# Optimization experiments

Measured on AMD Instinct MI355X. Metric: run time of the kernel, lower is better.

The kernel has to match this reference:

```python
import jax, jax.numpy as jnp
import numpy as np
from jax import lax

S, B, F = 512, 256, 128
HC = 256  # constraint LSTM hidden
HG = 256  # generation LSTM hidden
L = 128   # linear units


def _lstm_step(Wih, Whh, bias):
    """torch.nn.LSTMCell semantics: gates = x@Wih.T + h@Whh.T + bih + bhh,
    chunked as (i, f, g, o)."""
    def step(carry, x):
        h, c = carry
        gates = x @ Wih.T + h @ Whh.T + bias
        i, f, g, o = jnp.split(gates, 4, axis=-1)
        c2 = jax.nn.sigmoid(f) * c + jax.nn.sigmoid(i) * jnp.tanh(g)
        h2 = jax.nn.sigmoid(o) * jnp.tanh(c2)
        return (h2, c2), h2
    return step


def setup_inputs() -> dict:
    key = jax.random.key(0)
    ks = jax.random.split(key, 16)
    s = 0.05
    return {
        "seq": jax.random.normal(ks[0], (S, B, F), jnp.float32),
        "seq_constraints": jax.random.normal(ks[1], (S, B, F + 1), jnp.float32),
        "Wih_c": jax.random.normal(ks[2], (4 * HC, F + 1), jnp.float32) * s,
        "Whh_c": jax.random.normal(ks[3], (4 * HC, HC), jnp.float32) * s,
        "bih_c": jax.random.normal(ks[4], (4 * HC,), jnp.float32) * s,
        "bhh_c": jax.random.normal(ks[5], (4 * HC,), jnp.float32) * s,
        "Wih_g": jax.random.normal(ks[6], (4 * HG, F + HC), jnp.float32) * s,
        "Whh_g": jax.random.normal(ks[7], (4 * HG, HG), jnp.float32) * s,
        "bih_g": jax.random.normal(ks[8], (4 * HG,), jnp.float32) * s,
        "bhh_g": jax.random.normal(ks[9], (4 * HG,), jnp.float32) * s,
        "W1": jax.random.normal(ks[10], (L, HG), jnp.float32) * s,
        "b1": jax.random.normal(ks[11], (L,), jnp.float32) * s,
        "W2": jax.random.normal(ks[12], (F, L), jnp.float32) * s,
        "b2": jax.random.normal(ks[13], (F,), jnp.float32) * s,
    }


def reference(seq, seq_constraints, Wih_c, Whh_c, bih_c, bhh_c,
              Wih_g, Whh_g, bih_g, bhh_g, W1, b1, W2, b2):
    seq_len, batch, nf = seq.shape
    dt = seq.dtype

    # --- constraint LSTM, scanned backward in time; outputs aligned to time index ---
    step_c = _lstm_step(Wih_c, Whh_c, bih_c + bhh_c)
    z_c = jnp.zeros((batch, HC), dt)
    _, hc = lax.scan(step_c, (z_c, z_c), seq_constraints, reverse=True)  # (S,B,HC)

    # --- generation LSTM input: seq shifted right by one step (zeros at t=0),
    #     concatenated with the constraint hidden at time t ---
    shifted = jnp.concatenate([jnp.zeros((1, batch, nf), dt), seq[:-1]], axis=0)
    gen_in = jnp.concatenate([shifted, hc], axis=-1)  # (S,B,F+HC)

    step_g = _lstm_step(Wih_g, Whh_g, bih_g + bhh_g)
    z_g = jnp.zeros((batch, HG), dt)
    _, hg = lax.scan(step_g, (z_g, z_g), gen_in)  # (S,B,HG)

    # --- per-step MLP head ---
    preds = jax.nn.relu(hg @ W1.T + b1) @ W2.T + b2  # (S,B,F)
    return preds
```

## Files before the change

### kernel.cpp

```cpp
#include <hip/hip_runtime.h>

typedef unsigned short u16;
typedef unsigned int u32;
typedef unsigned long long u64;
typedef __attribute__((ext_vector_type(8))) short s16x8;
typedef __attribute__((ext_vector_type(4))) float f32x4;

#define MFMA_BF16 __builtin_amdgcn_mfma_f32_16x16x32_bf16

#define TCH 64
#define NCH 8
#define CROWS (TCH * 256)

__device__ __forceinline__ float b2f(u16 u) {
  u32 v = ((u32)u) << 16; float f; __builtin_memcpy(&f, &v, 4); return f;
}
__device__ __forceinline__ u16 f2b(float f) {
  u32 u; __builtin_memcpy(&u, &f, 4);
  u += 0x7FFFu + ((u >> 16) & 1u);
  return (u16)(u >> 16);
}
__device__ __forceinline__ float sigm(float x) {
  float e = __builtin_amdgcn_exp2f(-1.44269504f * x);
  return __builtin_amdgcn_rcpf(1.0f + e);
}
__device__ __forceinline__ float tanh_(float x) {
  float e = __builtin_amdgcn_exp2f(2.88539008f * x);
  return 1.0f - 2.0f * __builtin_amdgcn_rcpf(e + 1.0f);
}

__global__ void prep_weights(const float* __restrict__ Wihc, const float* __restrict__ Whhc,
                             const float* __restrict__ bihc, const float* __restrict__ bhhc,
                             const float* __restrict__ Wihg, const float* __restrict__ Whhg,
                             const float* __restrict__ bihg, const float* __restrict__ bhhg,
                             const float* __restrict__ W1, const float* __restrict__ W2,
                             u16* __restrict__ pWihc, u16* __restrict__ pWhhc,
                             u16* __restrict__ pWihg, u16* __restrict__ pWhhg,
                             u16* __restrict__ pW1, u16* __restrict__ pW2,
                             float* __restrict__ pbc, float* __restrict__ pbg) {
  const int b = blockIdx.x, t = threadIdx.x;
  if (b < 1024) { if (t < 192) pWihc[b * 192 + t] = (t < 129) ? f2b(Wihc[b * 129 + t]) : (u16)0; }
  else if (b < 2048) { int n = b - 1024; pWhhc[n * 256 + t] = f2b(Whhc[n * 256 + t]); }
  else if (b < 3072) { int n = b - 2048; for (int k = t; k < 384; k += 256) pWihg[n * 384 + k] = f2b(Wihg[n * 384 + k]); }
  else if (b < 4096) { int n = b - 3072; pWhhg[n * 256 + t] = f2b(Whhg[n * 256 + t]); }
  else if (b < 4224) { int n = b - 4096; pW1[n * 256 + t] = f2b(W1[n * 256 + t]); }
  else if (b < 4352) { int n = b - 4224; if (t < 128) pW2[n * 128 + t] = f2b(W2[n * 128 + t]); }
  else {
    int i = (b - 4352) * 256 + t;
    if (i < 1024) pbc[i] = bihc[i] + bhhc[i];
    else if (i < 2048) pbg[i - 1024] = bihg[i - 1024] + bhhg[i - 1024];
  }
}

__global__ void conv_scb(const float* __restrict__ src, u16* __restrict__ dst, int r0) {
  const int row = blockIdx.x, t = threadIdx.x;
  dst[(size_t)row * 192 + t] = (t < 129) ? f2b(src[(size_t)(r0 + row) * 129 + t]) : (u16)0;
}
__global__ void conv_seqb(const float* __restrict__ src, u16* __restrict__ dst, int r0) {
  const int row = blockIdx.x, t = threadIdx.x;
  const int g = r0 + row;
  dst[(size_t)row * 128 + t] = (g < 256) ? (u16)0 : f2b(src[(size_t)(g - 256) * 128 + t]);
}

__global__ void fill_val(float* __restrict__ p, float v, int n) {
  int i = blockIdx.x * 256 + threadIdx.x;
  if (i < n) p[i] = v;
}

template <int RELU, int OUTF32>
__global__ __launch_bounds__(256, 1) void gemm_bias(
    const u16* __restrict__ A1, int lda1, const u16* __restrict__ A2, int lda2,
    const u16* __restrict__ Bw, const float* __restrict__ bias,
    void* __restrict__ Outv, int N) {
  const int K = lda1 + lda2;
  const int ntiles = N >> 7;
  const int bm = blockIdx.x / ntiles, bn = blockIdx.x % ntiles;
  const int m0 = bm << 7, n0 = bn << 7;
  __shared__ u16 Al[128 * 64], Bl[128 * 64];
  const int tid = threadIdx.x, lane = tid & 63, w = tid >> 6;
  const int kg = lane >> 4, l15 = lane & 15;
  const int mq = (w & 1) << 6, nq = (w >> 1) << 6;

  f32x4 acc[4][4];
#pragma unroll
  for (int mt = 0; mt < 4; ++mt)
#pragma unroll
    for (int nt = 0; nt < 4; ++nt) acc[mt][nt] = (f32x4){0.f, 0.f, 0.f, 0.f};

#pragma unroll 1
  for (int kc = 0; kc < K; kc += 64) {
#pragma unroll
    for (int i = 0; i < 4; ++i) {
      int id = i * 256 + tid;
      int row = id >> 3;
      int c8 = (id & 7) * 8;
      int k = kc + c8;
      const u16* asrc = (k < lda1) ? (A1 + (size_t)(m0 + row) * lda1 + k)
                                   : (A2 + (size_t)(m0 + row) * lda2 + (k - lda1));
      s16x8 av = *(const s16x8*)asrc;
      s16x8 bv = *(const s16x8*)(Bw + (size_t)(n0 + row) * K + k);
      int sw = (row & 7) << 3;
      *(s16x8*)&Al[row * 64 + (c8 ^ sw)] = av;
      *(s16x8*)&Bl[row * 64 + (c8 ^ sw)] = bv;
    }
    __syncthreads();
#pragma unroll
    for (int kk = 0; kk < 2; ++kk) {
      const int kb = kk * 32 + kg * 8;
      s16x8 a[4], b[4];
#pragma unroll
      for (int mt = 0; mt < 4; ++mt) {
        int r = mq + mt * 16 + l15;
        a[mt] = *(const s16x8*)&Al[r * 64 + (kb ^ ((r & 7) << 3))];
      }
#pragma unroll
      for (int nt = 0; nt < 4; ++nt) {
        int r = nq + nt * 16 + l15;
        b[nt] = *(const s16x8*)&Bl[r * 64 + (kb ^ ((r & 7) << 3))];
      }
#pragma unroll
      for (int mt = 0; mt < 4; ++mt)
#pragma unroll
        for (int nt = 0; nt < 4; ++nt)
          acc[mt][nt] = MFMA_BF16(a[mt], b[nt], acc[mt][nt], 0, 0, 0);
    }
    __syncthreads();
  }
#pragma unroll
  for (int nt = 0; nt < 4; ++nt) {
    const int col = n0 + nq + nt * 16 + l15;
    const float bb = bias[col];
#pragma unroll
    for (int mt = 0; mt < 4; ++mt)
#pragma unroll
      for (int r = 0; r < 4; ++r) {
        float v = acc[mt][nt][r] + bb;
        if (RELU) v = fmaxf(v, 0.f);
        const size_t orow = (size_t)(m0 + mq + mt * 16 + kg * 4 + r);
        if (OUTF32) ((float*)Outv)[orow * N + col] = v;
        else ((u16*)Outv)[orow * N + col] = f2b(v);
      }
  }
}

__global__ __launch_bounds__(256, 1) void lstm_scan(
    const u16* __restrict__ X,
    const u16* __restrict__ Whh,
    u16* __restrict__ Hc,
    const u16* __restrict__ ph,
    float* __restrict__ Cst,
    u64* __restrict__ HX,
    u32* __restrict__ slots,
    int base, int fwd, int first) {
  __shared__ u16 hlds[32 * 256];
  const int tid = threadIdx.x;
  const int lane = tid & 63;
  const int w = tid >> 6;
  const int bg = blockIdx.x & 7;
  const int hs = blockIdx.x >> 3;
  const int kg = lane >> 4;
  const int l15 = lane & 15;
  const int mrow = (w & 1) * 16;
  const int rowL = mrow + l15;
  const int brow = bg * 32 + rowL;
  const int hcol0 = hs * 32 + (w >> 1) * 16 + kg * 4;
  u32* myslot = slots + ((bg << 3) + hs) * 32;

  s16x8 breg[4][8];
  const int wrow = hs * 32 + (w >> 1) * 16 + l15;
#pragma unroll
  for (int q = 0; q < 4; ++q)
#pragma unroll
    for (int kt = 0; kt < 8; ++kt)
      breg[q][kt] = *(const s16x8*)&Whh[(size_t)(q * 256 + wrow) * 256 + kt * 32 + kg * 8];

  if (first) {
#pragma unroll
    for (int i = 0; i < 8; ++i) {
      int idx = i * 256 + tid;
      int row = idx >> 6, c0 = (idx & 63) * 4;
      *(u64*)&hlds[row * 256 + (c0 ^ ((row & 7) << 3))] = 0ull;
    }
  } else {
    const u64* hsrc = (const u64*)ph + bg * 2048;
#pragma unroll
    for (int i = 0; i < 8; ++i) {
      int idx = i * 256 + tid;
      int row = idx >> 6, c0 = (idx & 63) * 4;
      u64 v = hsrc[idx];
      *(u64*)&hlds[row * 256 + (c0 ^ ((row & 7) << 3))] = v;
    }
  }
  float c4[4];
  if (first) {
    c4[0] = 0.f; c4[1] = 0.f; c4[2] = 0.f; c4[3] = 0.f;
  } else {
    f32x4 cv = *(const f32x4*)&Cst[(size_t)brow * 256 + hcol0];
    c4[0] = cv[0]; c4[1] = cv[1]; c4[2] = cv[2]; c4[3] = cv[3];
  }
  __syncthreads();

  u64 xv[4];
  {
    const int lt0 = fwd ? 0 : TCH - 1;
    const u16* xb = X + ((size_t)lt0 * 256 + brow) * 1024 + hcol0;
#pragma unroll
    for (int q = 0; q < 4; ++q) xv[q] = *(const u64*)(xb + q * 256);
  }

  const int abase = rowL * 256;
  const int aswz = (rowL & 7) << 3;
  const int widx = (w >> 1) * 4 + kg;
  const int rrow = tid >> 3;
  const int ridx = tid & 7;

#pragma unroll 1
  for (int s = 0; s < TCH; ++s) {
    const int lt = fwd ? s : TCH - 1 - s;
    const u32 tag = (u32)(base + s + 1);
    u64* slab = HX + ((size_t)(s & 1) * 8 + bg) * 2048;

    f32x4 acc[2][4];
#pragma unroll
    for (int p = 0; p < 2; ++p)
#pragma unroll
      for (int q = 0; q < 4; ++q) acc[p][q] = (f32x4){0.f, 0.f, 0.f, 0.f};

#pragma unroll
    for (int kt = 0; kt < 8; ++kt) {
      s16x8 hb = *(const s16x8*)&hlds[abase + ((kt * 32 + kg * 8) ^ aswz)];
#pragma unroll
      for (int q = 0; q < 4; ++q)
        acc[kt & 1][q] = MFMA_BF16(breg[q][kt], hb, acc[kt & 1][q], 0, 0, 0);
    }

    u16 hb16[4];
    u64 hu = 0;
#pragma unroll
    for (int r = 0; r < 4; ++r) {
      float gi = acc[0][0][r] + acc[1][0][r] + b2f((u16)(xv[0] >> (16 * r)));
      float gf = acc[0][1][r] + acc[1][1][r] + b2f((u16)(xv[1] >> (16 * r)));
      float gg = acc[0][2][r] + acc[1][2][r] + b2f((u16)(xv[2] >> (16 * r)));
      float go = acc[0][3][r] + acc[1][3][r] + b2f((u16)(xv[3] >> (16 * r)));
      float cn = sigm(gf) * c4[r] + sigm(gi) * tanh_(gg);
      c4[r] = cn;
      hb16[r] = f2b(sigm(go) * tanh_(cn));
      hu |= ((u64)hb16[r]) << (16 * r);
    }

    if (s == TCH - 1) {
      *(u64*)&Hc[((size_t)lt * 256 + brow) * 256 + hcol0] = hu;
      break;
    }

    __hip_atomic_store(slab + ((size_t)hs * 32 + rowL) * 8 + widx, hu,
                       __ATOMIC_RELAXED, __HIP_MEMORY_SCOPE_AGENT);
    __syncthreads();

    if (tid == 0)
      __hip_atomic_store(myslot, tag, __ATOMIC_RELAXED, __HIP_MEMORY_SCOPE_AGENT);

    *(u64*)&Hc[((size_t)lt * 256 + brow) * 256 + hcol0] = hu;
    {
      const int nlt = fwd ? lt + 1 : lt - 1;
      const u16* xb = X + ((size_t)nlt * 256 + brow) * 1024 + hcol0;
#pragma unroll
      for (int q = 0; q < 4; ++q) xv[q] = *(const u64*)(xb + q * 256);
    }
    __builtin_amdgcn_sched_barrier(0);

    if (w == 0 && lane < 8) {
      const u32* sp = slots + ((bg << 3) + lane) * 32;
      int guard = 0;
      while (__hip_atomic_load(sp, __ATOMIC_RELAXED, __HIP_MEMORY_SCOPE_AGENT) < tag &&
             guard < (1 << 16)) {
        __builtin_amdgcn_s_sleep(1);
        ++guard;
      }
    }
    __builtin_amdgcn_s_barrier();

    u64 pv[8];
#pragma unroll
    for (int k = 0; k < 8; ++k)
      pv[k] = __hip_atomic_load(slab + k * 256 + tid,
                                __ATOMIC_RELAXED, __HIP_MEMORY_SCOPE_AGENT);
#pragma unroll
    for (int k = 0; k < 8; ++k) {
      int c = k * 32 + ridx * 4;
      *(u64*)&hlds[rrow * 256 + (c ^ ((rrow & 7) << 3))] = pv[k];
    }
    __syncthreads();
  }

  f32x4 cv; cv[0] = c4[0]; cv[1] = c4[1]; cv[2] = c4[2]; cv[3] = c4[3];
  *(f32x4*)&Cst[(size_t)brow * 256 + hcol0] = cv;
}

extern "C" void kernel_launch(void* const* d_in, const int* in_sizes, int n_in,
                              void* d_out, int out_size, void* d_ws, size_t ws_size,
                              hipStream_t stream) {
  (void)in_sizes; (void)n_in;
  const float* seq  = (const float*)d_in[0];
  const float* sc   = (const float*)d_in[1];
  const float* Wihc = (const float*)d_in[2];
  const float* Whhc = (const float*)d_in[3];
  const float* bihc = (const float*)d_in[4];
  const float* bhhc = (const float*)d_in[5];
  const float* Wihg = (const float*)d_in[6];
  const float* Whhg = (const float*)d_in[7];
  const float* bihg = (const float*)d_in[8];
  const float* bhhg = (const float*)d_in[9];
  const float* W1   = (const float*)d_in[10];
  const float* b1   = (const float*)d_in[11];
  const float* W2   = (const float*)d_in[12];
  const float* b2   = (const float*)d_in[13];

  char* ws = (char*)d_ws;
  const size_t o_Xbuf = 0;
  const size_t o_scbc = o_Xbuf + (size_t)CROWS * 1024 * 2;
  const size_t o_seqc = o_scbc + (size_t)CROWS * 192 * 2;
  const size_t o_hgc  = o_seqc + (size_t)CROWS * 128 * 2;
  const size_t o_t1c  = o_hgc  + (size_t)CROWS * 256 * 2;
  const size_t o_Wihc = o_t1c  + (size_t)CROWS * 128 * 2;
  const size_t o_Whhc = o_Wihc + 1024 * 192 * 2;
  const size_t o_Wihg = o_Whhc + 1024 * 256 * 2;
  const size_t o_Whhg = o_Wihg + 1024 * 384 * 2;
  const size_t o_W1   = o_Whhg + 1024 * 256 * 2;
  const size_t o_W2   = o_W1   + 128 * 256 * 2;
  const size_t o_bc   = o_W2   + 128 * 128 * 2;
  const size_t o_bg   = o_bc   + 1024 * 4;
  const size_t o_Cst  = o_bg   + 1024 * 4;
  const size_t o_HX   = o_Cst  + 256 * 256 * 4;
  const size_t o_slt  = o_HX   + (size_t)2 * 8 * 2048 * 8;
  const size_t NEEDED = o_slt + 64 * 128;

  if (ws_size < NEEDED) {
    fill_val<<<(out_size + 255) / 256, 256, 0, stream>>>((float*)d_out, 1.0e6f, out_size);
    return;
  }

  u16* Xbuf  = (u16*)(ws + o_Xbuf);
  u16* scbc  = (u16*)(ws + o_scbc);
  u16* seqc  = (u16*)(ws + o_seqc);
  u16* hgc   = (u16*)(ws + o_hgc);
  u16* t1c   = (u16*)(ws + o_t1c);
  u16* pWihc = (u16*)(ws + o_Wihc);
  u16* pWhhc = (u16*)(ws + o_Whhc);
  u16* pWihg = (u16*)(ws + o_Wihg);
  u16* pWhhg = (u16*)(ws + o_Whhg);
  u16* pW1   = (u16*)(ws + o_W1);
  u16* pW2   = (u16*)(ws + o_W2);
  float* pbc = (float*)(ws + o_bc);
  float* pbg = (float*)(ws + o_bg);
  float* Cst = (float*)(ws + o_Cst);
  u64* HX    = (u64*)(ws + o_HX);
  u32* slots = (u32*)(ws + o_slt);

  u16* hcb = (u16*)d_out;

  hipMemsetAsync(slots, 0, 64 * 128, stream);
  prep_weights<<<4360, 256, 0, stream>>>(Wihc, Whhc, bihc, bhhc, Wihg, Whhg, bihg, bhhg,
                                         W1, W2, pWihc, pWhhc, pWihg, pWhhg, pW1, pW2, pbc, pbg);

  for (int c = NCH - 1; c >= 0; --c) {
    const int r0 = c * CROWS;
    conv_scb<<<CROWS, 192, 0, stream>>>(sc, scbc, r0);
    gemm_bias<0, 0><<<(CROWS / 128) * 8, 256, 0, stream>>>(scbc, 192, scbc, 0, pWihc, pbc, Xbuf, 1024);
    u16* Hcp = hcb + (size_t)c * TCH * 65536;
    const u16* ph = (c == NCH - 1) ? (const u16*)0 : hcb + (size_t)(c + 1) * TCH * 65536;
    const int ord = NCH - 1 - c;
    lstm_scan<<<64, 256, 0, stream>>>(Xbuf, pWhhc, Hcp, ph, Cst, HX, slots,
                                      ord * TCH, 0, c == NCH - 1);
  }

  for (int c = 0; c < NCH; ++c) {
    const int r0 = c * CROWS;
    conv_seqb<<<CROWS, 128, 0, stream>>>(seq, seqc, r0);
    const u16* hcc = hcb + (size_t)c * TCH * 65536;
    gemm_bias<0, 0><<<(CROWS / 128) * 8, 256, 0, stream>>>(seqc, 128, hcc, 256, pWihg, pbg, Xbuf, 1024);
    const u16* ph = (c == 0) ? (const u16*)0 : hgc + (size_t)(TCH - 1) * 65536;
    const int ord = NCH + c;
    lstm_scan<<<64, 256, 0, stream>>>(Xbuf, pWhhg, hgc, ph, Cst, HX, slots,
                                      ord * TCH, 1, c == 0);
    gemm_bias<1, 0><<<CROWS / 128, 256, 0, stream>>>(hgc, 256, hgc, 0, pW1, b1, t1c, 128);
    gemm_bias<0, 1><<<CROWS / 128, 256, 0, stream>>>(t1c, 128, t1c, 0, pW2, b2,
                                                     (float*)d_out + (size_t)c * CROWS * 128, 128);
  }
}
```

Measured before the change: 2.820 ms.

## Replace block-level LDS h exchange with per-wave flags and direct register loads

```diff
diff --git a/kernel.cpp b/kernel.cpp
--- a/kernel.cpp
+++ b/kernel.cpp
@@ -152,7 +152,6 @@
     u64* __restrict__ HX,
     u32* __restrict__ slots,
     int base, int fwd, int first) {
-  __shared__ u16 hlds[32 * 256];
   const int tid = threadIdx.x;
   const int lane = tid & 63;
   const int w = tid >> 6;
@@ -164,7 +163,8 @@
   const int rowL = mrow + l15;
   const int brow = bg * 32 + rowL;
   const int hcol0 = hs * 32 + (w >> 1) * 16 + kg * 4;
-  u32* myslot = slots + ((bg << 3) + hs) * 32;
+  u32* myslot = slots + ((bg << 3) + hs) * 32 + w;
+  const u32* pollp = slots + ((bg << 3) + (lane >> 2)) * 32 + (lane & 3);
 
   s16x8 breg[4][8];
   const int wrow = hs * 32 + (w >> 1) * 16 + l15;
@@ -174,23 +174,16 @@
     for (int kt = 0; kt < 8; ++kt)
       breg[q][kt] = *(const s16x8*)&Whh[(size_t)(q * 256 + wrow) * 256 + kt * 32 + kg * 8];
 
+  s16x8 hreg[8];
   if (first) {
 #pragma unroll
-    for (int i = 0; i < 8; ++i) {
-      int idx = i * 256 + tid;
-      int row = idx >> 6, c0 = (idx & 63) * 4;
-      *(u64*)&hlds[row * 256 + (c0 ^ ((row & 7) << 3))] = 0ull;
-    }
+    for (int kt = 0; kt < 8; ++kt) hreg[kt] = (s16x8){0, 0, 0, 0, 0, 0, 0, 0};
   } else {
-    const u64* hsrc = (const u64*)ph + bg * 2048;
-#pragma unroll
-    for (int i = 0; i < 8; ++i) {
-      int idx = i * 256 + tid;
-      int row = idx >> 6, c0 = (idx & 63) * 4;
-      u64 v = hsrc[idx];
-      *(u64*)&hlds[row * 256 + (c0 ^ ((row & 7) << 3))] = v;
-    }
-  }
+#pragma unroll
+    for (int kt = 0; kt < 8; ++kt)
+      hreg[kt] = *(const s16x8*)&ph[(size_t)brow * 256 + kt * 32 + kg * 8];
+  }
+
   float c4[4];
   if (first) {
     c4[0] = 0.f; c4[1] = 0.f; c4[2] = 0.f; c4[3] = 0.f;
@@ -198,7 +191,6 @@
     f32x4 cv = *(const f32x4*)&Cst[(size_t)brow * 256 + hcol0];
     c4[0] = cv[0]; c4[1] = cv[1]; c4[2] = cv[2]; c4[3] = cv[3];
   }
-  __syncthreads();
 
   u64 xv[4];
   {
@@ -208,17 +200,11 @@
     for (int q = 0; q < 4; ++q) xv[q] = *(const u64*)(xb + q * 256);
   }
 
-  const int abase = rowL * 256;
-  const int aswz = (rowL & 7) << 3;
-  const int widx = (w >> 1) * 4 + kg;
-  const int rrow = tid >> 3;
-  const int ridx = tid & 7;
-
 #pragma unroll 1
   for (int s = 0; s < TCH; ++s) {
     const int lt = fwd ? s : TCH - 1 - s;
     const u32 tag = (u32)(base + s + 1);
-    u64* slab = HX + ((size_t)(s & 1) * 8 + bg) * 2048;
+    u16* slab16 = (u16*)HX + (((size_t)(s & 1) * 8 + bg) << 13);
 
     f32x4 acc[2][4];
 #pragma unroll
@@ -228,10 +214,9 @@
 
 #pragma unroll
     for (int kt = 0; kt < 8; ++kt) {
-      s16x8 hb = *(const s16x8*)&hlds[abase + ((kt * 32 + kg * 8) ^ aswz)];
 #pragma unroll
       for (int q = 0; q < 4; ++q)
-        acc[kt & 1][q] = MFMA_BF16(breg[q][kt], hb, acc[kt & 1][q], 0, 0, 0);
+        acc[kt & 1][q] = MFMA_BF16(breg[q][kt], hreg[kt], acc[kt & 1][q], 0, 0, 0);
     }
 
     u16 hb16[4];
@@ -248,49 +233,44 @@
       hu |= ((u64)hb16[r]) << (16 * r);
     }
 
-    if (s == TCH - 1) {
-      *(u64*)&Hc[((size_t)lt * 256 + brow) * 256 + hcol0] = hu;
-      break;
-    }
-
-    __hip_atomic_store(slab + ((size_t)hs * 32 + rowL) * 8 + widx, hu,
+    *(u64*)&Hc[((size_t)lt * 256 + brow) * 256 + hcol0] = hu;
+    if (s == TCH - 1) break;
+
+    __hip_atomic_store((u64*)&slab16[(size_t)rowL * 256 + hcol0], hu,
                        __ATOMIC_RELAXED, __HIP_MEMORY_SCOPE_AGENT);
-    __syncthreads();
-
-    if (tid == 0)
+    __builtin_amdgcn_sched_barrier(0);
+    asm volatile("s_waitcnt vmcnt(0)" ::: "memory");
+    __builtin_amdgcn_sched_barrier(0);
+    if (lane == 0)
       __hip_atomic_store(myslot, tag, __ATOMIC_RELAXED, __HIP_MEMORY_SCOPE_AGENT);
 
-    *(u64*)&Hc[((size_t)lt * 256 + brow) * 256 + hcol0] = hu;
+    {
+      int guard = 0;
+      u32 v;
+      do {
+        v = (lane < 32)
+                ? __hip_atomic_load(pollp, __ATOMIC_RELAXED, __HIP_MEMORY_SCOPE_AGENT)
+                : tag;
+      } while (__any(v < tag) && ++guard < (1 << 15));
+    }
+    __builtin_amdgcn_sched_barrier(0);
+
+#pragma unroll
+    for (int kt = 0; kt < 8; ++kt) {
+      const u64* p = (const u64*)&slab16[(size_t)rowL * 256 + kt * 32 + kg * 8];
+      u64 a = __hip_atomic_load(p + 0, __ATOMIC_RELAXED, __HIP_MEMORY_SCOPE_AGENT);
+      u64 b = __hip_atomic_load(p + 1, __ATOMIC_RELAXED, __HIP_MEMORY_SCOPE_AGENT);
+      u64* hp = (u64*)&hreg[kt];
+      hp[0] = a; hp[1] = b;
+    }
+    __builtin_amdgcn_sched_barrier(0);
+
     {
       const int nlt = fwd ? lt + 1 : lt - 1;
       const u16* xb = X + ((size_t)nlt * 256 + brow) * 1024 + hcol0;
 #pragma unroll
       for (int q = 0; q < 4; ++q) xv[q] = *(const u64*)(xb + q * 256);
     }
-    __builtin_amdgcn_sched_barrier(0);
-
-    if (w == 0 && lane < 8) {
-      const u32* sp = slots + ((bg << 3) + lane) * 32;
-      int guard = 0;
-      while (__hip_atomic_load(sp, __ATOMIC_RELAXED, __HIP_MEMORY_SCOPE_AGENT) < tag &&
-             guard < (1 << 16)) {
-        __builtin_amdgcn_s_sleep(1);
-        ++guard;
-      }
-    }
-    __builtin_amdgcn_s_barrier();
-
-    u64 pv[8];
-#pragma unroll
-    for (int k = 0; k < 8; ++k)
-      pv[k] = __hip_atomic_load(slab + k * 256 + tid,
-                                __ATOMIC_RELAXED, __HIP_MEMORY_SCOPE_AGENT);
-#pragma unroll
-    for (int k = 0; k < 8; ++k) {
-      int c = k * 32 + ridx * 4;
-      *(u64*)&hlds[rrow * 256 + (c ^ ((rrow & 7) << 3))] = pv[k];
-    }
-    __syncthreads();
   }
 
   f32x4 cv; cv[0] = c4[0]; cv[1] = c4[1]; cv[2] = c4[2]; cv[3] = c4[3];
```

Measured after the change: 5.706 ms. 102% more time.

## Overlap next-chunk gate GEMM and MLP head with LSTM scan in one launch

Applied to the files above, without the earlier changes.

```diff
diff --git a/kernel.cpp b/kernel.cpp
--- a/kernel.cpp
+++ b/kernel.cpp
@@ -52,31 +52,19 @@
   }
 }
 
-__global__ void conv_scb(const float* __restrict__ src, u16* __restrict__ dst, int r0) {
-  const int row = blockIdx.x, t = threadIdx.x;
-  dst[(size_t)row * 192 + t] = (t < 129) ? f2b(src[(size_t)(r0 + row) * 129 + t]) : (u16)0;
-}
-__global__ void conv_seqb(const float* __restrict__ src, u16* __restrict__ dst, int r0) {
-  const int row = blockIdx.x, t = threadIdx.x;
-  const int g = r0 + row;
-  dst[(size_t)row * 128 + t] = (g < 256) ? (u16)0 : f2b(src[(size_t)(g - 256) * 128 + t]);
-}
-
 __global__ void fill_val(float* __restrict__ p, float v, int n) {
   int i = blockIdx.x * 256 + threadIdx.x;
   if (i < n) p[i] = v;
 }
 
-template <int RELU, int OUTF32>
-__global__ __launch_bounds__(256, 1) void gemm_bias(
-    const u16* __restrict__ A1, int lda1, const u16* __restrict__ A2, int lda2,
+template <int MODE>
+__device__ __forceinline__ void gate_gemm_tile(
+    int tile, int r0, const float* __restrict__ F, const u16* __restrict__ Hb,
     const u16* __restrict__ Bw, const float* __restrict__ bias,
-    void* __restrict__ Outv, int N) {
-  const int K = lda1 + lda2;
-  const int ntiles = N >> 7;
-  const int bm = blockIdx.x / ntiles, bn = blockIdx.x % ntiles;
+    u16* __restrict__ Out, u16* Al, u16* Bl) {
+  const int K = (MODE == 1) ? 192 : 384;
+  const int bm = tile >> 3, bn = tile & 7;
   const int m0 = bm << 7, n0 = bn << 7;
-  __shared__ u16 Al[128 * 64], Bl[128 * 64];
   const int tid = threadIdx.x, lane = tid & 63, w = tid >> 6;
   const int kg = lane >> 4, l15 = lane & 15;
   const int mq = (w & 1) << 6, nq = (w >> 1) << 6;
@@ -95,9 +83,29 @@
       int row = id >> 3;
       int c8 = (id & 7) * 8;
       int k = kc + c8;
-      const u16* asrc = (k < lda1) ? (A1 + (size_t)(m0 + row) * lda1 + k)
-                                   : (A2 + (size_t)(m0 + row) * lda2 + (k - lda1));
-      s16x8 av = *(const s16x8*)asrc;
+      s16x8 av;
+      if (MODE == 1) {
+        const float* s = F + (size_t)(r0 + m0 + row) * 129 + k;
+#pragma unroll
+        for (int j = 0; j < 8; ++j) {
+          u16 bb = 0;
+          if (k + j < 129) bb = f2b(s[j]);
+          av[j] = (short)bb;
+        }
+      } else {
+        if (k < 128) {
+          const int grow = r0 + m0 + row;
+          if (grow < 256) {
+            av = (s16x8){0, 0, 0, 0, 0, 0, 0, 0};
+          } else {
+            const float* s = F + (size_t)(grow - 256) * 128 + k;
+#pragma unroll
+            for (int j = 0; j < 8; ++j) av[j] = (short)f2b(s[j]);
+          }
+        } else {
+          av = *(const s16x8*)&Hb[(size_t)(m0 + row) * 256 + (k - 128)];
+        }
+      }
       s16x8 bv = *(const s16x8*)(Bw + (size_t)(n0 + row) * K + k);
       int sw = (row & 7) << 3;
       *(s16x8*)&Al[row * 64 + (c8 ^ sw)] = av;
@@ -134,25 +142,126 @@
     for (int mt = 0; mt < 4; ++mt)
 #pragma unroll
       for (int r = 0; r < 4; ++r) {
+        const size_t orow = (size_t)(m0 + mq + mt * 16 + kg * 4 + r);
+        Out[orow * 1024 + col] = f2b(acc[mt][nt][r] + bb);
+      }
+  }
+}
+
+template <int MODE>
+__global__ __launch_bounds__(256, 1) void gate_gemm_k(
+    int r0, const float* __restrict__ F, const u16* __restrict__ Hb,
+    const u16* __restrict__ Bw, const float* __restrict__ bias,
+    u16* __restrict__ Out) {
+  __shared__ u16 Al[8192], Bl[8192];
+  gate_gemm_tile<MODE>(blockIdx.x, r0, F, Hb, Bw, bias, Out, Al, Bl);
+}
+
+template <int RELU, int OUTF32>
+__device__ __forceinline__ void head_tile(
+    int tile, const u16* __restrict__ A, int lda,
+    const u16* __restrict__ Bw, const float* __restrict__ bias,
+    void* __restrict__ Outv, u16* Al, u16* Bl) {
+  const int m0 = tile << 7;
+  const int tid = threadIdx.x, lane = tid & 63, w = tid >> 6;
+  const int kg = lane >> 4, l15 = lane & 15;
+  const int mq = (w & 1) << 6, nq = (w >> 1) << 6;
+
+  f32x4 acc[4][4];
+#pragma unroll
+  for (int mt = 0; mt < 4; ++mt)
+#pragma unroll
+    for (int nt = 0; nt < 4; ++nt) acc[mt][nt] = (f32x4){0.f, 0.f, 0.f, 0.f};
+
+#pragma unroll 1
+  for (int kc = 0; kc < lda; kc += 64) {
+#pragma unroll
+    for (int i = 0; i < 4; ++i) {
+      int id = i * 256 + tid;
+      int row = id >> 3;
+      int c8 = (id & 7) * 8;
+      int k = kc + c8;
+      s16x8 av = *(const s16x8*)(A + (size_t)(m0 + row) * lda + k);
+      s16x8 bv = *(const s16x8*)(Bw + (size_t)row * lda + k);
+      int sw = (row & 7) << 3;
+      *(s16x8*)&Al[row * 64 + (c8 ^ sw)] = av;
+      *(s16x8*)&Bl[row * 64 + (c8 ^ sw)] = bv;
+    }
+    __syncthreads();
+#pragma unroll
+    for (int kk = 0; kk < 2; ++kk) {
+      const int kb = kk * 32 + kg * 8;
+      s16x8 a[4], b[4];
+#pragma unroll
+      for (int mt = 0; mt < 4; ++mt) {
+        int r = mq + mt * 16 + l15;
+        a[mt] = *(const s16x8*)&Al[r * 64 + (kb ^ ((r & 7) << 3))];
+      }
+#pragma unroll
+      for (int nt = 0; nt < 4; ++nt) {
+        int r = nq + nt * 16 + l15;
+        b[nt] = *(const s16x8*)&Bl[r * 64 + (kb ^ ((r & 7) << 3))];
+      }
+#pragma unroll
+      for (int mt = 0; mt < 4; ++mt)
+#pragma unroll
+        for (int nt = 0; nt < 4; ++nt)
+          acc[mt][nt] = MFMA_BF16(a[mt], b[nt], acc[mt][nt], 0, 0, 0);
+    }
+    __syncthreads();
+  }
+#pragma unroll
+  for (int nt = 0; nt < 4; ++nt) {
+    const int col = nq + nt * 16 + l15;
+    const float bb = bias[col];
+#pragma unroll
+    for (int mt = 0; mt < 4; ++mt)
+#pragma unroll
+      for (int r = 0; r < 4; ++r) {
         float v = acc[mt][nt][r] + bb;
         if (RELU) v = fmaxf(v, 0.f);
         const size_t orow = (size_t)(m0 + mq + mt * 16 + kg * 4 + r);
-        if (OUTF32) ((float*)Outv)[orow * N + col] = v;
-        else ((u16*)Outv)[orow * N + col] = f2b(v);
-      }
-  }
-}
-
+        if (OUTF32) ((float*)Outv)[orow * 128 + col] = v;
+        else ((u16*)Outv)[orow * 128 + col] = f2b(v);
+      }
+  }
+}
+
+template <int RELU, int OUTF32>
+__global__ __launch_bounds__(256, 1) void head_k(
+    const u16* __restrict__ A, int lda, const u16* __restrict__ Bw,
+    const float* __restrict__ bias, void* __restrict__ Outv) {
+  __shared__ u16 Al[8192], Bl[8192];
+  head_tile<RELU, OUTF32>(blockIdx.x, A, lda, Bw, bias, Outv, Al, Bl);
+}
+
+template <int GMODE>
 __global__ __launch_bounds__(256, 1) void lstm_scan(
-    const u16* __restrict__ X,
-    const u16* __restrict__ Whh,
-    u16* __restrict__ Hc,
-    const u16* __restrict__ ph,
-    float* __restrict__ Cst,
-    u64* __restrict__ HX,
-    u32* __restrict__ slots,
-    int base, int fwd, int first) {
-  __shared__ u16 hlds[32 * 256];
+    const u16* __restrict__ X, const u16* __restrict__ Whh,
+    u16* __restrict__ Hc, const u16* __restrict__ ph,
+    float* __restrict__ Cst, u64* __restrict__ HX, u32* __restrict__ slots,
+    int base, int fwd, int first,
+    const float* __restrict__ gF, const u16* __restrict__ gHb,
+    const u16* __restrict__ gBw, const float* __restrict__ gbias,
+    u16* __restrict__ gOut, int gr0, int ng,
+    const u16* __restrict__ h1A, u16* __restrict__ h1Out, int nh1,
+    const u16* __restrict__ h2A, float* __restrict__ h2Out, int nh2,
+    const u16* __restrict__ W1b, const float* __restrict__ b1,
+    const u16* __restrict__ W2b, const float* __restrict__ b2) {
+  __shared__ u16 lds[16384];
+  int bx = blockIdx.x;
+  if (bx >= 64) {
+    bx -= 64;
+    if (bx < ng) { gate_gemm_tile<GMODE>(bx, gr0, gF, gHb, gBw, gbias, gOut, lds, lds + 8192); return; }
+    bx -= ng;
+    if (bx < nh1) { head_tile<1, 0>(bx, h1A, 256, W1b, b1, (void*)h1Out, lds, lds + 8192); return; }
+    bx -= nh1;
+    if (bx < nh2) { head_tile<0, 1>(bx, h2A, 128, W2b, b2, (void*)h2Out, lds, lds + 8192); }
+    return;
+  }
+  __builtin_amdgcn_s_setprio(1);
+  u16* hlds = lds;
+
   const int tid = threadIdx.x;
   const int lane = tid & 63;
   const int w = tid >> 6;
@@ -164,7 +273,7 @@
   const int rowL = mrow + l15;
   const int brow = bg * 32 + rowL;
   const int hcol0 = hs * 32 + (w >> 1) * 16 + kg * 4;
-  u32* myslot = slots + ((bg << 3) + hs) * 32;
+  u32* myslot = slots + ((bg << 3) + hs) * 32 + w;
 
   s16x8 breg[4][8];
   const int wrow = hs * 32 + (w >> 1) * 16 + l15;
@@ -234,7 +343,6 @@
         acc[kt & 1][q] = MFMA_BF16(breg[q][kt], hb, acc[kt & 1][q], 0, 0, 0);
     }
 
-    u16 hb16[4];
     u64 hu = 0;
 #pragma unroll
     for (int r = 0; r < 4; ++r) {
@@ -244,23 +352,20 @@
       float go = acc[0][3][r] + acc[1][3][r] + b2f((u16)(xv[3] >> (16 * r)));
       float cn = sigm(gf) * c4[r] + sigm(gi) * tanh_(gg);
       c4[r] = cn;
-      hb16[r] = f2b(sigm(go) * tanh_(cn));
-      hu |= ((u64)hb16[r]) << (16 * r);
-    }
-
-    if (s == TCH - 1) {
-      *(u64*)&Hc[((size_t)lt * 256 + brow) * 256 + hcol0] = hu;
-      break;
-    }
-
+      hu |= ((u64)f2b(sigm(go) * tanh_(cn))) << (16 * r);
+    }
+
+    *(u64*)&Hc[((size_t)lt * 256 + brow) * 256 + hcol0] = hu;
+    if (s == TCH - 1) break;
     __hip_atomic_store(slab + ((size_t)hs * 32 + rowL) * 8 + widx, hu,
                        __ATOMIC_RELAXED, __HIP_MEMORY_SCOPE_AGENT);
-    __syncthreads();
-
-    if (tid == 0)
+
+    __builtin_amdgcn_sched_barrier(0);
+    asm volatile("s_waitcnt vmcnt(0)" ::: "memory");
+    __builtin_amdgcn_sched_barrier(0);
+    if (lane == 0)
       __hip_atomic_store(myslot, tag, __ATOMIC_RELAXED, __HIP_MEMORY_SCOPE_AGENT);
 
-    *(u64*)&Hc[((size_t)lt * 256 + brow) * 256 + hcol0] = hu;
     {
       const int nlt = fwd ? lt + 1 : lt - 1;
       const u16* xb = X + ((size_t)nlt * 256 + brow) * 1024 + hcol0;
@@ -269,11 +374,11 @@
     }
     __builtin_amdgcn_sched_barrier(0);
 
-    if (w == 0 && lane < 8) {
-      const u32* sp = slots + ((bg << 3) + lane) * 32;
+    if (w == 0 && lane < 32) {
+      const u32* sp = slots + ((bg << 3) + (lane >> 2)) * 32 + (lane & 3);
       int guard = 0;
       while (__hip_atomic_load(sp, __ATOMIC_RELAXED, __HIP_MEMORY_SCOPE_AGENT) < tag &&
-             guard < (1 << 16)) {
+             guard < (1 << 15)) {
         __builtin_amdgcn_s_sleep(1);
         ++guard;
       }
@@ -316,75 +421,103 @@
   const float* W2   = (const float*)d_in[12];
   const float* b2   = (const float*)d_in[13];
 
-  char* ws = (char*)d_ws;
-  const size_t o_Xbuf = 0;
-  const size_t o_scbc = o_Xbuf + (size_t)CROWS * 1024 * 2;
-  const size_t o_seqc = o_scbc + (size_t)CROWS * 192 * 2;
-  const size_t o_hgc  = o_seqc + (size_t)CROWS * 128 * 2;
-  const size_t o_t1c  = o_hgc  + (size_t)CROWS * 256 * 2;
-  const size_t o_Wihc = o_t1c  + (size_t)CROWS * 128 * 2;
-  const size_t o_Whhc = o_Wihc + 1024 * 192 * 2;
-  const size_t o_Wihg = o_Whhc + 1024 * 256 * 2;
-  const size_t o_Whhg = o_Wihg + 1024 * 384 * 2;
-  const size_t o_W1   = o_Whhg + 1024 * 256 * 2;
-  const size_t o_W2   = o_W1   + 128 * 256 * 2;
-  const size_t o_bc   = o_W2   + 128 * 128 * 2;
-  const size_t o_bg   = o_bc   + 1024 * 4;
-  const size_t o_Cst  = o_bg   + 1024 * 4;
-  const size_t o_HX   = o_Cst  + 256 * 256 * 4;
-  const size_t o_slt  = o_HX   + (size_t)2 * 8 * 2048 * 8;
-  const size_t NEEDED = o_slt + 64 * 128;
-
-  if (ws_size < NEEDED) {
+  const size_t XB = (size_t)CROWS * 1024 * 2;
+  const size_t HGB = (size_t)CROWS * 256 * 2;
+  const size_t T1B = (size_t)CROWS * 128 * 2;
+  const size_t TAILB = 1024 * 192 * 2 + 1024 * 256 * 2 + 1024 * 384 * 2 +
+                       1024 * 256 * 2 + 128 * 256 * 2 + 128 * 128 * 2 +
+                       1024 * 4 + 1024 * 4 + 256 * 256 * 4 +
+                       (size_t)2 * 8 * 2048 * 8 + 64 * 128;
+  const size_t NEED_BIG = 2 * XB + 2 * HGB + 2 * T1B + TAILB;
+  const size_t NEED_SMALL = XB + HGB + T1B + TAILB;
+  const int use2 = ws_size >= NEED_BIG;
+
+  if (ws_size < NEED_SMALL) {
     fill_val<<<(out_size + 255) / 256, 256, 0, stream>>>((float*)d_out, 1.0e6f, out_size);
     return;
   }
 
-  u16* Xbuf  = (u16*)(ws + o_Xbuf);
-  u16* scbc  = (u16*)(ws + o_scbc);
-  u16* seqc  = (u16*)(ws + o_seqc);
-  u16* hgc   = (u16*)(ws + o_hgc);
-  u16* t1c   = (u16*)(ws + o_t1c);
-  u16* pWihc = (u16*)(ws + o_Wihc);
-  u16* pWhhc = (u16*)(ws + o_Whhc);
-  u16* pWihg = (u16*)(ws + o_Wihg);
-  u16* pWhhg = (u16*)(ws + o_Whhg);
-  u16* pW1   = (u16*)(ws + o_W1);
-  u16* pW2   = (u16*)(ws + o_W2);
-  float* pbc = (float*)(ws + o_bc);
-  float* pbg = (float*)(ws + o_bg);
-  float* Cst = (float*)(ws + o_Cst);
-  u64* HX    = (u64*)(ws + o_HX);
-  u32* slots = (u32*)(ws + o_slt);
+  char* ws = (char*)d_ws;
+  size_t off = 0;
+  u16* Xh[2]; u16* hgb[2]; u16* t1b[2];
+  Xh[0] = (u16*)(ws + off); off += XB;
+  Xh[1] = use2 ? (u16*)(ws + off) : Xh[0]; if (use2) off += XB;
+  hgb[0] = (u16*)(ws + off); off += HGB;
+  hgb[1] = use2 ? (u16*)(ws + off) : hgb[0]; if (use2) off += HGB;
+  t1b[0] = (u16*)(ws + off); off += T1B;
+  t1b[1] = use2 ? (u16*)(ws + off) : t1b[0]; if (use2) off += T1B;
+  u16* pWihc = (u16*)(ws + off); off += 1024 * 192 * 2;
+  u16* pWhhc = (u16*)(ws + off); off += 1024 * 256 * 2;
+  u16* pWihg = (u16*)(ws + off); off += 1024 * 384 * 2;
+  u16* pWhhg = (u16*)(ws + off); off += 1024 * 256 * 2;
+  u16* pW1   = (u16*)(ws + off); off += 128 * 256 * 2;
+  u16* pW2   = (u16*)(ws + off); off += 128 * 128 * 2;
+  float* pbc = (float*)(ws + off); off += 1024 * 4;
+  float* pbg = (float*)(ws + off); off += 1024 * 4;
+  float* Cst = (float*)(ws + off); off += 256 * 256 * 4;
+  u64* HX    = (u64*)(ws + off); off += (size_t)2 * 8 * 2048 * 8;
+  u32* slots = (u32*)(ws + off);
 
   u16* hcb = (u16*)d_out;
+  float* outf = (float*)d_out;
 
   hipMemsetAsync(slots, 0, 64 * 128, stream);
   prep_weights<<<4360, 256, 0, stream>>>(Wihc, Whhc, bihc, bhhc, Wihg, Whhg, bihg, bhhg,
                                          W1, W2, pWihc, pWhhc, pWihg, pWhhg, pW1, pW2, pbc, pbg);
 
-  for (int c = NCH - 1; c >= 0; --c) {
-    const int r0 = c * CROWS;
-    conv_scb<<<CROWS, 192, 0, stream>>>(sc, scbc, r0);
-    gemm_bias<0, 0><<<(CROWS / 128) * 8, 256, 0, stream>>>(scbc, 192, scbc, 0, pWihc, pbc, Xbuf, 1024);
-    u16* Hcp = hcb + (size_t)c * TCH * 65536;
-    const u16* ph = (c == NCH - 1) ? (const u16*)0 : hcb + (size_t)(c + 1) * TCH * 65536;
-    const int ord = NCH - 1 - c;
-    lstm_scan<<<64, 256, 0, stream>>>(Xbuf, pWhhc, Hcp, ph, Cst, HX, slots,
-                                      ord * TCH, 0, c == NCH - 1);
-  }
-
-  for (int c = 0; c < NCH; ++c) {
-    const int r0 = c * CROWS;
-    conv_seqb<<<CROWS, 128, 0, stream>>>(seq, seqc, r0);
-    const u16* hcc = hcb + (size_t)c * TCH * 65536;
-    gemm_bias<0, 0><<<(CROWS / 128) * 8, 256, 0, stream>>>(seqc, 128, hcc, 256, pWihg, pbg, Xbuf, 1024);
-    const u16* ph = (c == 0) ? (const u16*)0 : hgc + (size_t)(TCH - 1) * 65536;
-    const int ord = NCH + c;
-    lstm_scan<<<64, 256, 0, stream>>>(Xbuf, pWhhg, hgc, ph, Cst, HX, slots,
-                                      ord * TCH, 1, c == 0);
-    gemm_bias<1, 0><<<CROWS / 128, 256, 0, stream>>>(hgc, 256, hgc, 0, pW1, b1, t1c, 128);
-    gemm_bias<0, 1><<<CROWS / 128, 256, 0, stream>>>(t1c, 128, t1c, 0, pW2, b2,
-                                                     (float*)d_out + (size_t)c * CROWS * 128, 128);
-  }
-}
+  if (use2) {
+    gate_gemm_k<1><<<1024, 256, 0, stream>>>(7 * CROWS, sc, (const u16*)0, pWihc, pbc, Xh[1]);
+    for (int c = NCH - 1; c >= 0; --c) {
+      const int ord = NCH - 1 - c;
+      const int ng = (c > 0) ? 1024 : 0;
+      u16* Hcp = hcb + (size_t)c * TCH * 65536;
+      const u16* ph = (c == NCH - 1) ? (const u16*)0 : hcb + (size_t)(c + 1) * TCH * 65536;
+      lstm_scan<1><<<64 + ng, 256, 0, stream>>>(
+          Xh[c & 1], pWhhc, Hcp, ph, Cst, HX, slots, ord * TCH, 0, c == NCH - 1,
+          sc, (const u16*)0, pWihc, pbc, Xh[(c - 1) & 1], (c - 1) * CROWS, ng,
+          (const u16*)0, (u16*)0, 0, (const u16*)0, (float*)0, 0, pW1, b1, pW2, b2);
+    }
+    gate_gemm_k<2><<<1024, 256, 0, stream>>>(0, seq, hcb, pWihg, pbg, Xh[0]);
+    for (int c = 0; c < NCH; ++c) {
+      const int ord = NCH + c;
+      const int ng = (c < NCH - 1) ? 1024 : 0;
+      const int nh1 = (c >= 1) ? 128 : 0;
+      const int nh2 = (c >= 2) ? 128 : 0;
+      const u16* ph = (c == 0) ? (const u16*)0 : hgb[(c - 1) & 1] + (size_t)(TCH - 1) * 65536;
+      lstm_scan<2><<<64 + ng + nh1 + nh2, 256, 0, stream>>>(
+          Xh[c & 1], pWhhg, hgb[c & 1], ph, Cst, HX, slots, ord * TCH, 1, c == 0,
+          seq, hcb + (size_t)(c + 1) * TCH * 65536, pWihg, pbg,
+          Xh[(c + 1) & 1], (c + 1) * CROWS, ng,
+          hgb[(c - 1) & 1], t1b[(c - 1) & 1], nh1,
+          t1b[c & 1], outf + (size_t)(c - 2) * CROWS * 128, nh2,
+          pW1, b1, pW2, b2);
+    }
+    head_k<1, 0><<<128, 256, 0, stream>>>(hgb[1], 256, pW1, b1, (void*)t1b[1]);
+    head_k<0, 1><<<128, 256, 0, stream>>>(t1b[0], 128, pW2, b2,
+                                          (void*)(outf + (size_t)6 * CROWS * 128));
+    head_k<0, 1><<<128, 256, 0, stream>>>(t1b[1], 128, pW2, b2,
+                                          (void*)(outf + (size_t)7 * CROWS * 128));
+  } else {
+    for (int c = NCH - 1; c >= 0; --c) {
+      gate_gemm_k<1><<<1024, 256, 0, stream>>>(c * CROWS, sc, (const u16*)0, pWihc, pbc, Xh[0]);
+      u16* Hcp = hcb + (size_t)c * TCH * 65536;
+      const u16* ph = (c == NCH - 1) ? (const u16*)0 : hcb + (size_t)(c + 1) * TCH * 65536;
+      lstm_scan<1><<<64, 256, 0, stream>>>(
+          Xh[0], pWhhc, Hcp, ph, Cst, HX, slots, (NCH - 1 - c) * TCH, 0, c == NCH - 1,
+          sc, (const u16*)0, pWihc, pbc, Xh[0], 0, 0,
+          (const u16*)0, (u16*)0, 0, (const u16*)0, (float*)0, 0, pW1, b1, pW2, b2);
+    }
+    for (int c = 0; c < NCH; ++c) {
+      gate_gemm_k<2><<<1024, 256, 0, stream>>>(c * CROWS, seq,
+                                               hcb + (size_t)c * TCH * 65536, pWihg, pbg, Xh[0]);
+      const u16* ph = (c == 0) ? (const u16*)0 : hgb[0] + (size_t)(TCH - 1) * 65536;
+      lstm_scan<2><<<64, 256, 0, stream>>>(
+          Xh[0], pWhhg, hgb[0], ph, Cst, HX, slots, (NCH + c) * TCH, 1, c == 0,
+          seq, (const u16*)0, pWihg, pbg, Xh[0], 0, 0,
+          (const u16*)0, (u16*)0, 0, (const u16*)0, (float*)0, 0, pW1, b1, pW2, b2);
+      head_k<1, 0><<<128, 256, 0, stream>>>(hgb[0], 256, pW1, b1, (void*)t1b[0]);
+      head_k<0, 1><<<128, 256, 0, stream>>>(t1b[0], 128, pW2, b2,
+                                            (void*)(outf + (size_t)c * CROWS * 128));
+    }
+  }
+}
```

After: 3.346 ms. 1.19x slower.

## Tag each exchanged hidden value with its step to allow per-word validation

Applied to the files above, without the earlier changes.

```diff
diff --git a/kernel.cpp b/kernel.cpp
--- a/kernel.cpp
+++ b/kernel.cpp
@@ -166,6 +166,10 @@
   const int hcol0 = hs * 32 + (w >> 1) * 16 + kg * 4;
   u32* myslot = slots + ((bg << 3) + hs) * 32;
 
+  const int rrow = tid >> 3;
+  const int rcol0 = (tid & 7) * 32;
+  const int rsw = (rrow & 7) << 3;
+
   s16x8 breg[4][8];
   const int wrow = hs * 32 + (w >> 1) * 16 + l15;
 #pragma unroll
@@ -210,15 +214,13 @@
 
   const int abase = rowL * 256;
   const int aswz = (rowL & 7) << 3;
-  const int widx = (w >> 1) * 4 + kg;
-  const int rrow = tid >> 3;
-  const int ridx = tid & 7;
 
 #pragma unroll 1
   for (int s = 0; s < TCH; ++s) {
     const int lt = fwd ? s : TCH - 1 - s;
     const u32 tag = (u32)(base + s + 1);
-    u64* slab = HX + ((size_t)(s & 1) * 8 + bg) * 2048;
+    const u64 tagpat = (u64)tag * 0x100000001ull;
+    u64* slab = HX + ((size_t)(s & 1) * 8 + bg) * 4096;
 
     f32x4 acc[2][4];
 #pragma unroll
@@ -253,10 +255,15 @@
       break;
     }
 
-    __hip_atomic_store(slab + ((size_t)hs * 32 + rowL) * 8 + widx, hu,
-                       __ATOMIC_RELAXED, __HIP_MEMORY_SCOPE_AGENT);
-    __syncthreads();
-
+    {
+      u64* wp = slab + (size_t)rowL * 128 + (hcol0 >> 1);
+      u64 w0 = (u64)(((u32)hb16[0] << 16) | tag) | ((u64)(((u32)hb16[1] << 16) | tag) << 32);
+      u64 w1 = (u64)(((u32)hb16[2] << 16) | tag) | ((u64)(((u32)hb16[3] << 16) | tag) << 32);
+      __hip_atomic_store(wp + 0, w0, __ATOMIC_RELAXED, __HIP_MEMORY_SCOPE_AGENT);
+      __hip_atomic_store(wp + 1, w1, __ATOMIC_RELAXED, __HIP_MEMORY_SCOPE_AGENT);
+    }
+    __builtin_amdgcn_sched_barrier(0);
+    __builtin_amdgcn_s_barrier();
     if (tid == 0)
       __hip_atomic_store(myslot, tag, __ATOMIC_RELAXED, __HIP_MEMORY_SCOPE_AGENT);
 
@@ -273,22 +280,38 @@
       const u32* sp = slots + ((bg << 3) + lane) * 32;
       int guard = 0;
       while (__hip_atomic_load(sp, __ATOMIC_RELAXED, __HIP_MEMORY_SCOPE_AGENT) < tag &&
-             guard < (1 << 16)) {
+             guard < (1 << 18)) {
         __builtin_amdgcn_s_sleep(1);
         ++guard;
       }
     }
     __builtin_amdgcn_s_barrier();
 
-    u64 pv[8];
-#pragma unroll
-    for (int k = 0; k < 8; ++k)
-      pv[k] = __hip_atomic_load(slab + k * 256 + tid,
-                                __ATOMIC_RELAXED, __HIP_MEMORY_SCOPE_AGENT);
-#pragma unroll
-    for (int k = 0; k < 8; ++k) {
-      int c = k * 32 + ridx * 4;
-      *(u64*)&hlds[rrow * 256 + (c ^ ((rrow & 7) << 3))] = pv[k];
+    u64 wv[16];
+    {
+      const u64* rp = slab + (size_t)rrow * 128 + (rcol0 >> 1);
+      int guard = 0;
+      for (;;) {
+#pragma unroll
+        for (int k = 0; k < 16; ++k)
+          wv[k] = __hip_atomic_load(rp + k, __ATOMIC_RELAXED, __HIP_MEMORY_SCOPE_AGENT);
+        u64 bad = 0;
+#pragma unroll
+        for (int k = 0; k < 16; ++k) bad |= (wv[k] ^ tagpat);
+        if ((bad & 0x0000FFFF0000FFFFull) == 0 || ++guard >= (1 << 14)) break;
+        __builtin_amdgcn_s_sleep(1);
+      }
+    }
+
+    {
+      u16* hrow = &hlds[rrow * 256];
+#pragma unroll
+      for (int j = 0; j < 8; ++j) {
+        u64 s0 = wv[2 * j], s1 = wv[2 * j + 1];
+        u64 o = ((s0 >> 16) & 0xFFFFull) | (((s0 >> 48) & 0xFFFFull) << 16)
+              | (((s1 >> 16) & 0xFFFFull) << 32) | ((s1 >> 48) << 48);
+        *(u64*)&hrow[(rcol0 + 4 * j) ^ rsw] = o;
+      }
     }
     __syncthreads();
   }
@@ -332,7 +355,7 @@
   const size_t o_bg   = o_bc   + 1024 * 4;
   const size_t o_Cst  = o_bg   + 1024 * 4;
   const size_t o_HX   = o_Cst  + 256 * 256 * 4;
-  const size_t o_slt  = o_HX   + (size_t)2 * 8 * 2048 * 8;
+  const size_t o_slt  = o_HX   + (size_t)2 * 8 * 4096 * 8;
   const size_t NEEDED = o_slt + 64 * 128;
 
   if (ws_size < NEEDED) {
@@ -359,6 +382,7 @@
 
   u16* hcb = (u16*)d_out;
 
+  hipMemsetAsync(HX, 0, (size_t)2 * 8 * 4096 * 8, stream);
   hipMemsetAsync(slots, 0, 64 * 128, stream);
   prep_weights<<<4360, 256, 0, stream>>>(Wihc, Whhc, bihc, bhhc, Wihg, Whhg, bihg, bhhg,
                                          W1, W2, pWihc, pWhhc, pWihg, pWhhg, pW1, pW2, pbc, pbg);
```

Measured after the change: 4.986 ms. 76.8% more time.
